# Kernel tuning notes

Measured on AMD Instinct MI355X. Metric: run time of the kernel, lower is better.

The kernel has to match this reference:

```python
import jax, jax.numpy as jnp
import numpy as np

EPS = 1e-5
TOP_K = 50

def _layernorm(h, g, b):
    mu = jnp.mean(h, axis=-1, keepdims=True)
    var = jnp.mean((h - mu) ** 2, axis=-1, keepdims=True)
    return (h - mu) * jax.lax.rsqrt(var + EPS) * g + b

def setup_inputs() -> dict:
    key = jax.random.key(0)
    ks = jax.random.split(key, 8)
    B, D, E = 16384, 384, 2048
    return {
        "x": jax.random.normal(ks[0], (B, D), jnp.float32),
        "We": jax.random.normal(ks[1], (D, E), jnp.float32) * 0.05,
        "be": jax.random.normal(ks[2], (E,), jnp.float32) * 0.01,
        "g1": jnp.ones((E,), jnp.float32),
        "b1": jnp.zeros((E,), jnp.float32),
        "Wd": jax.random.normal(ks[3], (E, D), jnp.float32) * 0.02,
        "bd": jax.random.normal(ks[4], (D,), jnp.float32) * 0.01,
        "Wb": jax.random.normal(ks[5], (E, D), jnp.float32) * 0.02,
        "bb": jax.random.normal(ks[6], (D,), jnp.float32) * 0.01,
        "g2": jnp.ones((D,), jnp.float32),
        "b2": jnp.zeros((D,), jnp.float32),
    }

def reference(x, We, be, g1, b1, Wd, bd, Wb, bb, g2, b2):
    # encoder: Linear -> LayerNorm -> ReLU
    h = jax.nn.relu(_layernorm(x @ We + be, g1, b1))  # [B, E]
    # top-k sparsification: zero all but top-50 per row (scatter mask, matches torch)
    _, idx = jax.lax.top_k(h, TOP_K)                  # [B, K]
    rows = jnp.arange(h.shape[0])[:, None]
    mask = jnp.zeros_like(h).at[rows, idx].set(1.0)
    sparse = h * mask                                 # [B, E]
    recon = sparse @ Wd + bd                          # [B, D]
    separated = _layernorm(sparse @ Wb + bb, g2, b2)  # [B, D]
    return recon, sparse, separated
```

## Files before the change

kernel.cpp:

```cpp
#include <hip/hip_runtime.h>
#include <hip/hip_bf16.h>
#include <stdint.h>

#define B_D   384
#define B_E   2048
#define TOPK  50
#define LN_EPS 1e-5f
#define NKP   12
#define FIX_WINDOW 2e-4f

typedef short bf16x8 __attribute__((ext_vector_type(8)));
typedef float f32x4  __attribute__((ext_vector_type(4)));

__device__ __forceinline__ float wave_sum_f(float v) {
#pragma unroll
    for (int d = 1; d < 64; d <<= 1) v += __shfl_xor(v, d, 64);
    return v;
}
__device__ __forceinline__ int wave_sum_i(int v) {
#pragma unroll
    for (int d = 1; d < 64; d <<= 1) v += __shfl_xor(v, d, 64);
    return v;
}
__device__ __forceinline__ float wave_max_f(float v) {
#pragma unroll
    for (int d = 1; d < 64; d <<= 1) v = fmaxf(v, __shfl_xor(v, d, 64));
    return v;
}

__device__ __forceinline__ ushort f2bf_hi(float v) {
    __hip_bfloat16 b = __float2bfloat16(v);
    return *(ushort*)&b;
}
__device__ __forceinline__ ushort f2bf_lo(float v) {
    __hip_bfloat16 b = __float2bfloat16(v);
    float rem = v - __bfloat162float(b);
    __hip_bfloat16 l = __float2bfloat16(rem);
    return *(ushort*)&l;
}

__device__ __forceinline__ void llds16(const void* g, void* l) {
    __builtin_amdgcn_global_load_lds((const __attribute__((address_space(1))) void*)g,
                                     (__attribute__((address_space(3))) void*)l, 16, 0, 0);
}

__global__ __launch_bounds__(256) void pack_AB(
    const float* __restrict__ x, const float* __restrict__ We,
    ushort* __restrict__ Ap, ushort* __restrict__ Bp, int* __restrict__ cntr)
{
    const int ks = blockIdx.x, yb = blockIdx.y, t = threadIdx.x;
    if (cntr && t == 0 && ks == 0 && yb == 0) *cntr = 0;
    if (yb < 64) {
        const int mt = yb;
#pragma unroll
        for (int q = 0; q < 8; ++q) {
            const int s = q * 256 + t;
            const int m = s & 255, kg = s >> 8;
            const int kp = ks * 64 + kg * 8;
            const int hi = (kp < 384);
            const int ksrc = hi ? kp : kp - 384;
            const float* src = x + (size_t)(mt * 256 + m) * B_D + ksrc;
            float4 v0 = *(const float4*)src;
            float4 v1 = *(const float4*)(src + 4);
            float vv[8] = {v0.x, v0.y, v0.z, v0.w, v1.x, v1.y, v1.z, v1.w};
            ushort o[8];
#pragma unroll
            for (int e = 0; e < 8; ++e)
                o[e] = hi ? f2bf_hi(vv[e]) : f2bf_lo(vv[e]);
            *(uint4*)(Ap + ((size_t)(mt * NKP + ks) * 2048 + s) * 8) = *(uint4*)o;
        }
    } else {
        const int nt = yb - 64;
#pragma unroll
        for (int q = 0; q < 8; ++q) {
            const int s = q * 256 + t;
            const int nl = s & 255, kg = s >> 8;
            const int kp = ks * 64 + kg * 8;
            const int hi = (kp < 384);
            const int ksrc = hi ? kp : kp - 384;
            const int ng = nt * 256 + nl;
            ushort o[8];
#pragma unroll
            for (int e = 0; e < 8; ++e) {
                float v = We[(size_t)(ksrc + e) * B_E + ng];
                o[e] = hi ? f2bf_hi(v) : f2bf_lo(v);
            }
            *(uint4*)(Bp + ((size_t)(nt * NKP + ks) * 2048 + s) * 8) = *(uint4*)o;
        }
    }
}

__global__ __launch_bounds__(512, 2) void enc_mfma256b(
    const ushort* __restrict__ Ap, const ushort* __restrict__ Bp,
    const float* __restrict__ be, float* __restrict__ y)
{
    __shared__ __align__(16) ushort Ah[2][8192];
    __shared__ __align__(16) ushort Al[2][8192];
    __shared__ __align__(16) ushort Bh[2][8192];
    __shared__ __align__(16) ushort Bl[2][8192];
    const int t = threadIdx.x, lane = t & 63, w = t >> 6;
    const int wr = w >> 2, wc = w & 3;
    const int gid = blockIdx.x;
    const int swz = (gid & 7) * 64 + (gid >> 3);
    const int nt = swz & 7, mt = swz >> 3;
    const ushort* gA = Ap + (size_t)mt * NKP * 16384;
    const ushort* gB = Bp + (size_t)nt * NKP * 16384;

    f32x4 acc[8][4];
#pragma unroll
    for (int i = 0; i < 8; ++i)
#pragma unroll
        for (int j = 0; j < 4; ++j)
#pragma unroll
            for (int r = 0; r < 4; ++r) acc[i][j][r] = 0.f;

    const int l15 = lane & 15, l4 = lane >> 4;

#define STAGEH(hk_, b_)                                                         \
    {                                                                           \
        const int hh = (hk_);                                                   \
        const int kt = hh >> 1, hf = hh & 1;                                    \
        const ushort* ah_ = gA + (size_t)kt * 16384 + hf * 8192 + t * 8;        \
        const ushort* al_ = gA + (size_t)(kt + 6) * 16384 + hf * 8192 + t * 8;  \
        const ushort* bh_ = gB + (size_t)kt * 16384 + hf * 8192 + t * 8;        \
        const ushort* bl_ = gB + (size_t)(kt + 6) * 16384 + hf * 8192 + t * 8;  \
        llds16(ah_,        &Ah[b_][t * 8]);                                     \
        llds16(ah_ + 4096, &Ah[b_][4096 + t * 8]);                              \
        llds16(al_,        &Al[b_][t * 8]);                                     \
        llds16(al_ + 4096, &Al[b_][4096 + t * 8]);                              \
        llds16(bh_,        &Bh[b_][t * 8]);                                     \
        llds16(bh_ + 4096, &Bh[b_][4096 + t * 8]);                              \
        llds16(bl_,        &Bl[b_][t * 8]);                                     \
        llds16(bl_ + 4096, &Bl[b_][4096 + t * 8]);                              \
    }

    STAGEH(0, 0);
    __syncthreads();

    for (int hk = 0; hk < 12; ++hk) {
        const int sl = hk & 1;
        if (hk + 1 < 12) STAGEH(hk + 1, sl ^ 1);
        bf16x8 bhf[4], ahf[8];
#pragma unroll
        for (int j = 0; j < 4; ++j)
            bhf[j] = *(const bf16x8*)&Bh[sl][(l4 * 256 + wc * 64 + j * 16 + l15) * 8];
#pragma unroll
        for (int i = 0; i < 8; ++i)
            ahf[i] = *(const bf16x8*)&Ah[sl][(l4 * 256 + wr * 128 + i * 16 + l15) * 8];
#pragma unroll
        for (int i = 0; i < 8; ++i)
#pragma unroll
            for (int j = 0; j < 4; ++j)
                acc[i][j] = __builtin_amdgcn_mfma_f32_16x16x32_bf16(ahf[i], bhf[j], acc[i][j], 0, 0, 0);
        bf16x8 blf[4];
#pragma unroll
        for (int j = 0; j < 4; ++j)
            blf[j] = *(const bf16x8*)&Bl[sl][(l4 * 256 + wc * 64 + j * 16 + l15) * 8];
#pragma unroll
        for (int i = 0; i < 8; ++i)
#pragma unroll
            for (int j = 0; j < 4; ++j)
                acc[i][j] = __builtin_amdgcn_mfma_f32_16x16x32_bf16(ahf[i], blf[j], acc[i][j], 0, 0, 0);
        bf16x8 alf[8];
#pragma unroll
        for (int i = 0; i < 8; ++i)
            alf[i] = *(const bf16x8*)&Al[sl][(l4 * 256 + wr * 128 + i * 16 + l15) * 8];
#pragma unroll
        for (int i = 0; i < 8; ++i)
#pragma unroll
            for (int j = 0; j < 4; ++j)
                acc[i][j] = __builtin_amdgcn_mfma_f32_16x16x32_bf16(alf[i], bhf[j], acc[i][j], 0, 0, 0);
        if (hk + 1 < 12) __syncthreads();
    }
#undef STAGEH

    float bev[4];
#pragma unroll
    for (int j = 0; j < 4; ++j) bev[j] = be[nt * 256 + wc * 64 + j * 16 + l15];
#pragma unroll
    for (int i = 0; i < 8; ++i)
#pragma unroll
        for (int j = 0; j < 4; ++j)
#pragma unroll
            for (int r = 0; r < 4; ++r) {
                const int row = mt * 256 + wr * 128 + i * 16 + l4 * 4 + r;
                const int col = nt * 256 + wc * 64 + j * 16 + l15;
                y[(size_t)row * B_E + col] = acc[i][j][r] + bev[j];
            }
}

__global__ __launch_bounds__(256) void enc_gemm_f32(
    const float* __restrict__ x, const float* __restrict__ We,
    const float* __restrict__ be, float* __restrict__ y)
{
    __shared__ float As[8][128];
    __shared__ float Bs[8][128];
    const int t  = threadIdx.x;
    const int m0 = blockIdx.y * 128;
    const int n0 = blockIdx.x * 128;
    const int tx = t & 15, ty = t >> 4;
    const int la_m = t >> 1, la_k = (t & 1) * 4;
    const int lb_k = t >> 5, lb_c = (t & 31) * 4;

    float acc[8][8];
#pragma unroll
    for (int i = 0; i < 8; ++i)
#pragma unroll
        for (int j = 0; j < 8; ++j) acc[i][j] = 0.f;

    for (int k0 = 0; k0 < B_D; k0 += 8) {
        float4 a = *(const float4*)&x[(size_t)(m0 + la_m) * B_D + k0 + la_k];
        float4 b = *(const float4*)&We[(size_t)(k0 + lb_k) * B_E + n0 + lb_c];
        __syncthreads();
        As[la_k + 0][la_m] = a.x;
        As[la_k + 1][la_m] = a.y;
        As[la_k + 2][la_m] = a.z;
        As[la_k + 3][la_m] = a.w;
        *(float4*)&Bs[lb_k][lb_c] = b;
        __syncthreads();
#pragma unroll
        for (int kk = 0; kk < 8; ++kk) {
            float4 a0 = *(const float4*)&As[kk][ty * 4];
            float4 a1 = *(const float4*)&As[kk][ty * 4 + 64];
            float4 b0 = *(const float4*)&Bs[kk][tx * 4];
            float4 b1 = *(const float4*)&Bs[kk][tx * 4 + 64];
            float av[8] = {a0.x,a0.y,a0.z,a0.w,a1.x,a1.y,a1.z,a1.w};
            float bv[8] = {b0.x,b0.y,b0.z,b0.w,b1.x,b1.y,b1.z,b1.w};
#pragma unroll
            for (int i = 0; i < 8; ++i)
#pragma unroll
                for (int j = 0; j < 8; ++j)
                    acc[i][j] = fmaf(av[i], bv[j], acc[i][j]);
        }
    }
    float4 beL = *(const float4*)&be[n0 + tx * 4];
    float4 beH = *(const float4*)&be[n0 + 64 + tx * 4];
    float bl[8] = {beL.x,beL.y,beL.z,beL.w,beH.x,beH.y,beH.z,beH.w};
#pragma unroll
    for (int i = 0; i < 8; ++i) {
        int row = m0 + ty * 4 + (i & 3) + (i >> 2) * 64;
        float4 o0 = {acc[i][0]+bl[0], acc[i][1]+bl[1], acc[i][2]+bl[2], acc[i][3]+bl[3]};
        float4 o1 = {acc[i][4]+bl[4], acc[i][5]+bl[5], acc[i][6]+bl[6], acc[i][7]+bl[7]};
        *(float4*)&y[(size_t)row * B_E + n0 + tx * 4]      = o0;
        *(float4*)&y[(size_t)row * B_E + n0 + 64 + tx * 4] = o1;
    }
}

__device__ __forceinline__ int ln_topk_row(
    float (&h)[32], int lane, const float* __restrict__ g1, const float* __restrict__ b1,
    float* __restrict__ row, int* __restrict__ IwR, float* __restrict__ VwR,
    float* __restrict__ ldsv, int* __restrict__ ldsi)
{
    float s = 0.f;
#pragma unroll
    for (int j = 0; j < 32; ++j) s += h[j];
    s = wave_sum_f(s);
    const float mu = s * (1.f / B_E);
    float ss = 0.f;
#pragma unroll
    for (int j = 0; j < 32; ++j) { float d = h[j] - mu; ss += d * d; }
    ss = wave_sum_f(ss);
    const float rstd = rsqrtf(ss * (1.f / B_E) + LN_EPS);
#pragma unroll
    for (int q = 0; q < 8; ++q) {
        float4 g  = *(const float4*)&g1[q * 256 + lane * 4];
        float4 bb = *(const float4*)&b1[q * 256 + lane * 4];
        float gg[4]  = {g.x,g.y,g.z,g.w};
        float bbv[4] = {bb.x,bb.y,bb.z,bb.w};
#pragma unroll
        for (int i = 0; i < 4; ++i) {
            int j = q*4+i;
            h[j] = fmaxf(fmaf((h[j] - mu) * rstd, gg[i], bbv[i]), 0.f);
        }
    }
    float mx = h[0];
#pragma unroll
    for (int j = 1; j < 32; ++j) mx = fmaxf(mx, h[j]);
    mx = wave_max_f(mx);

    float vlo = 0.f, vhi = __uint_as_float(__float_as_uint(mx) + 1u);
    int cl = 2048;
    bool window = false;
    for (int it = 0; it < 20; ++it) {
        float mid = 0.5f * (vlo + vhi);
        if (it == 0 && 2.2f > vlo && 2.2f < vhi) mid = 2.2f;
        if (!(mid > vlo && mid < vhi)) break;
        int c = 0;
#pragma unroll
        for (int j = 0; j < 32; ++j)
            c += (int)__popcll(__ballot(h[j] >= mid));
        if (c >= TOPK) { vlo = mid; cl = c; if (c <= 64) { window = true; break; } }
        else vhi = mid;
    }
    unsigned lo = __float_as_uint(vlo);
    if (!window) {
        unsigned hi = __float_as_uint(vhi);
        while (hi - lo > 1u) {
            const unsigned mid = lo + ((hi - lo) >> 1);
            const float mf = __uint_as_float(mid);
            int c = 0;
#pragma unroll
            for (int j = 0; j < 32; ++j)
                c += (int)__popcll(__ballot(h[j] >= mf));
            if (c >= TOPK) { lo = mid; cl = c; if (c <= 64) break; }
            else hi = mid;
        }
    }
    const float T0 = __uint_as_float(lo);

    unsigned selmask = 0u;
    int flag = 0;
    bool fastSel = (cl <= 64 && T0 > 0.f);

    if (fastSel) {
        ldsv[lane] = -1.f;
        ldsi[lane] = 1 << 20;
        asm volatile("s_waitcnt lgkmcnt(0)" ::: "memory");
        int base = 0;
#pragma unroll
        for (int j = 0; j < 32; ++j) {
            const bool p = (h[j] >= T0);
            const unsigned long long m = __ballot(p);
            if (p) {
                const int pos = base + (int)__popcll(m & ((1ull << lane) - 1ull));
                ldsv[pos] = h[j];
                ldsi[pos] = (j >> 2) * 256 + lane * 4 + (j & 3);
            }
            base += (int)__popcll(m);
        }
        asm volatile("s_waitcnt lgkmcnt(0)" ::: "memory");
        float sv = ldsv[lane];
        int   si = ldsi[lane];
#pragma unroll
        for (int k = 2; k <= 64; k <<= 1) {
#pragma unroll
            for (int jj = k >> 1; jj > 0; jj >>= 1) {
                const float ov = __shfl_xor(sv, jj, 64);
                const int   oi = __shfl_xor(si, jj, 64);
                const bool dirUp = ((lane & k) == 0);
                const bool lower = ((lane & jj) == 0);
                const bool mineBefore = (sv > ov) || (sv == ov && si < oi);
                const bool keep = (lower == dirUp) ? mineBefore : !mineBefore;
                if (!keep) { sv = ov; si = oi; }
            }
        }
        const float T    = __shfl(sv, TOPK - 1, 64);
        const int   idxT = __shfl(si, TOPK - 1, 64);
        float v51;
        if (cl > TOPK) {
            v51 = __shfl(sv, TOPK, 64);
        } else {
            float bb = -1.f;
#pragma unroll
            for (int j = 0; j < 32; ++j) bb = (h[j] < T0) ? fmaxf(bb, h[j]) : bb;
            v51 = wave_max_f(bb);
        }
        flag = (T - v51 < FIX_WINDOW) ? 1 : 0;
#pragma unroll
        for (int j = 0; j < 32; ++j) {
            const int e = (j >> 2) * 256 + lane * 4 + (j & 3);
            if (h[j] > T || (h[j] == T && e <= idxT)) selmask |= (1u << j);
        }
        if (lane < TOPK) { IwR[lane] = si; VwR[lane] = sv; }
    } else {
        const float T = T0;
        int cgt = 0, ceq = 0;
        float below = -1.f;
#pragma unroll
        for (int j = 0; j < 32; ++j) {
            cgt += (h[j] > T); ceq += (h[j] == T);
            if (h[j] < T) below = fmaxf(below, h[j]);
        }
        const int cgt_t = wave_sum_i(cgt);
        const int ceq_t = wave_sum_i(ceq);
        below = wave_max_f(below);
        const int need = TOPK - cgt_t;

        if (cgt_t + ceq_t == TOPK) {
#pragma unroll
            for (int j = 0; j < 32; ++j) if (h[j] >= T) selmask |= (1u << j);
        } else {
            int base = 0;
            for (int q = 0; q < 8; ++q) {
                int tc = 0;
#pragma unroll
                for (int i = 0; i < 4; ++i) tc += (h[q*4+i] == T);
                int ip = tc;
#pragma unroll
                for (int d = 1; d < 64; d <<= 1) {
                    int o = __shfl_up(ip, d, 64);
                    if (lane >= d) ip += o;
                }
                int rk  = base + ip - tc;
                int tot = __shfl(ip, 63, 64);
#pragma unroll
                for (int i = 0; i < 4; ++i) {
                    int j = q*4+i;
                    if (h[j] > T) selmask |= (1u << j);
                    else if (h[j] == T) { if (rk < need) selmask |= (1u << j); rk++; }
                }
                base += tot;
            }
        }
        if (T > 0.f) {
            if (cgt_t + ceq_t != TOPK && ceq_t > need) flag = 1;
            else if (T - below < FIX_WINDOW) flag = 1;
        }
        const int myc = __popc(selmask);
        int ip = myc;
#pragma unroll
        for (int d = 1; d < 64; d <<= 1) {
            int o = __shfl_up(ip, d, 64);
            if (lane >= d) ip += o;
        }
        int pos = ip - myc;
        for (int j = 0; j < 32; ++j) {
            if ((selmask >> j) & 1u) {
                int e = (j >> 2) * 256 + lane * 4 + (j & 3);
                IwR[pos] = e;
                VwR[pos] = h[j];
                pos++;
            }
        }
    }

#pragma unroll
    for (int q = 0; q < 8; ++q) {
        float4 o;
        o.x = ((selmask >> (q*4+0)) & 1u) ? h[q*4+0] : 0.f;
        o.y = ((selmask >> (q*4+1)) & 1u) ? h[q*4+1] : 0.f;
        o.z = ((selmask >> (q*4+2)) & 1u) ? h[q*4+2] : 0.f;
        o.w = ((selmask >> (q*4+3)) & 1u) ? h[q*4+3] : 0.f;
        *(float4*)&row[q * 256 + lane * 4] = o;
    }
    return flag;
}

__global__ __launch_bounds__(256) void topk_packW(
    float* __restrict__ y, const float* __restrict__ g1, const float* __restrict__ b1,
    int* __restrict__ Iw, float* __restrict__ Vw,
    int* __restrict__ rowlist, int* __restrict__ cntr,
    const float* __restrict__ Wd, const float* __restrict__ Wb, uint* __restrict__ Wp,
    int nTopk)
{
    __shared__ float ldsv[4][64];
    __shared__ int   ldsi[4][64];
    const int bid = blockIdx.x;
    const int t = threadIdx.x;
    if (bid >= nTopk) {
        const int e = (bid - nTopk) * 2 + (t >> 7);
        const int tt = t & 127;
#pragma unroll
        for (int j = 0; j < 3; ++j) {
            const int c = tt + 128 * j;
            const ushort d = f2bf_hi(Wd[(size_t)e * B_D + c]);
            const ushort b = f2bf_hi(Wb[(size_t)e * B_D + c]);
            Wp[(size_t)e * B_D + c] = ((uint)b << 16) | (uint)d;
        }
        return;
    }
    const int lane = t & 63;
    const int w = t >> 6;
    const int r = bid * 4 + w;
    float* row = y + (size_t)r * B_E;
    float h[32];
#pragma unroll
    for (int q = 0; q < 8; ++q) {
        float4 v = *(const float4*)&row[q * 256 + lane * 4];
        h[q*4+0] = v.x; h[q*4+1] = v.y; h[q*4+2] = v.z; h[q*4+3] = v.w;
    }
    int flag = ln_topk_row(h, lane, g1, b1, row, Iw + r * TOPK, Vw + r * TOPK,
                           ldsv[w], ldsi[w]);
    if (rowlist && lane == 0 && flag) {
        int p = atomicAdd(cntr, 1);
        rowlist[p] = r;
    }
}

__global__ __launch_bounds__(256) void fixup_recompute(
    const float* __restrict__ x, const float* __restrict__ We, const float* __restrict__ be,
    float* __restrict__ y, const int* __restrict__ rowlist, const int* __restrict__ cntr)
{
    const int nflag = *cntr;
    const int t = threadIdx.x;
    __shared__ float xs[8][B_D];
    __shared__ int   rIdx[8];

    for (int rb = blockIdx.y * 8; rb < nflag; rb += gridDim.y * 8) {
        const int nact = min(nflag - rb, 8);
        __syncthreads();
        if (t < 8) rIdx[t] = (t < nact) ? rowlist[rb + t] : -1;
        __syncthreads();
#pragma unroll
        for (int i = 0; i < 8; ++i) {
            if (i < nact) {
                const float* src = x + (size_t)rIdx[i] * B_D;
                for (int j = t; j < B_D; j += 256) xs[i][j] = src[j];
            } else {
                for (int j = t; j < B_D; j += 256) xs[i][j] = 0.f;
            }
        }
        __syncthreads();

        const int c = blockIdx.x * 256 + t;
        const float bc = be[c];
        float acc[8];
#pragma unroll
        for (int i = 0; i < 8; ++i) acc[i] = bc;
#pragma unroll 4
        for (int k = 0; k < B_D; ++k) {
            const float w = We[(size_t)k * B_E + c];
#pragma unroll
            for (int i = 0; i < 8; ++i) acc[i] = fmaf(xs[i][k], w, acc[i]);
        }
#pragma unroll
        for (int i = 0; i < 8; ++i)
            if (i < nact) y[(size_t)rIdx[i] * B_E + c] = acc[i];
    }
}

__global__ __launch_bounds__(256) void fixup_select(
    float* __restrict__ y, const float* __restrict__ g1, const float* __restrict__ b1,
    int* __restrict__ Iw, float* __restrict__ Vw,
    const int* __restrict__ rowlist, const int* __restrict__ cntr)
{
    __shared__ float ldsv[4][64];
    __shared__ int   ldsi[4][64];
    const int nflag = *cntr;
    const int w = threadIdx.x >> 6;
    const int lane = threadIdx.x & 63;
    for (int i = blockIdx.x * 4 + w; i < nflag; i += gridDim.x * 4) {
        const int r = rowlist[i];
        float* row = y + (size_t)r * B_E;
        float h[32];
#pragma unroll
        for (int q = 0; q < 8; ++q) {
            float4 v = *(const float4*)&row[q * 256 + lane * 4];
            h[q*4+0] = v.x; h[q*4+1] = v.y; h[q*4+2] = v.z; h[q*4+3] = v.w;
        }
        ln_topk_row(h, lane, g1, b1, row, Iw + r * TOPK, Vw + r * TOPK,
                    ldsv[w], ldsi[w]);
    }
}

__global__ __launch_bounds__(512) void decode_packed4(
    const int* __restrict__ Iw, const float* __restrict__ Vw,
    const uint* __restrict__ Wp, const float* __restrict__ bd,
    const float* __restrict__ bbias, const float* __restrict__ g2,
    const float* __restrict__ b2, float* __restrict__ recon, float* __restrict__ sep)
{
    __shared__ int   sI[4][TOPK];
    __shared__ float sV[4][TOPK];
    __shared__ float red[4][2];
    const int q = threadIdx.x >> 7;
    const int t = threadIdx.x & 127;
    const int r = blockIdx.x * 4 + q;
    if (t < TOPK) { sI[q][t] = Iw[r * TOPK + t]; sV[q][t] = Vw[r * TOPK + t]; }
    __syncthreads();
    float ad[3], ab[3];
#pragma unroll
    for (int j = 0; j < 3; ++j) { ad[j] = bd[t + 128*j]; ab[j] = bbias[t + 128*j]; }
#pragma unroll 2
    for (int i = 0; i < TOPK; ++i) {
        const int   idx = sI[q][i];
        const float v   = sV[q][i];
        const uint* wp  = Wp + (size_t)idx * B_D;
#pragma unroll
        for (int j = 0; j < 3; ++j) {
            const uint u = wp[t + 128*j];
            const float wd = __uint_as_float(u << 16);
            const float wb = __uint_as_float(u & 0xFFFF0000u);
            ad[j] = fmaf(v, wd, ad[j]);
            ab[j] = fmaf(v, wb, ab[j]);
        }
    }
#pragma unroll
    for (int j = 0; j < 3; ++j) recon[(size_t)r * B_D + t + 128*j] = ad[j];
    float s = ab[0] + ab[1] + ab[2];
    s = wave_sum_f(s);
    if ((t & 63) == 0) red[q][t >> 6] = s;
    __syncthreads();
    const float mu = (red[q][0] + red[q][1]) * (1.f / B_D);
    __syncthreads();
    float ss = 0.f;
#pragma unroll
    for (int j = 0; j < 3; ++j) { float d = ab[j] - mu; ss += d * d; }
    ss = wave_sum_f(ss);
    if ((t & 63) == 0) red[q][t >> 6] = ss;
    __syncthreads();
    const float rstd = rsqrtf((red[q][0] + red[q][1]) * (1.f / B_D) + LN_EPS);
#pragma unroll
    for (int j = 0; j < 3; ++j) {
        int c = t + 128*j;
        sep[(size_t)r * B_D + c] = fmaf((ab[j] - mu) * rstd, g2[c], b2[c]);
    }
}

__global__ __launch_bounds__(128) void decode_f32(
    const int* __restrict__ Iw, const float* __restrict__ Vw,
    const float* __restrict__ Wd, const float* __restrict__ bd,
    const float* __restrict__ Wb, const float* __restrict__ bbias,
    const float* __restrict__ g2, const float* __restrict__ b2,
    float* __restrict__ recon, float* __restrict__ sep)
{
    __shared__ int   sI[TOPK];
    __shared__ float sV[TOPK];
    __shared__ float red[2];
    const int r = blockIdx.x, t = threadIdx.x;
    if (t < TOPK) { sI[t] = Iw[r * TOPK + t]; sV[t] = Vw[r * TOPK + t]; }
    __syncthreads();
    float ad[3], ab[3];
#pragma unroll
    for (int j = 0; j < 3; ++j) { ad[j] = bd[t + 128*j]; ab[j] = bbias[t + 128*j]; }
#pragma unroll 2
    for (int i = 0; i < TOPK; ++i) {
        const int   idx = sI[i];
        const float v   = sV[i];
        const float* wd = Wd + (size_t)idx * B_D;
        const float* wb = Wb + (size_t)idx * B_D;
#pragma unroll
        for (int j = 0; j < 3; ++j) {
            ad[j] = fmaf(v, wd[t + 128*j], ad[j]);
            ab[j] = fmaf(v, wb[t + 128*j], ab[j]);
        }
    }
#pragma unroll
    for (int j = 0; j < 3; ++j) recon[(size_t)r * B_D + t + 128*j] = ad[j];
    float s = ab[0] + ab[1] + ab[2];
    s = wave_sum_f(s);
    if ((t & 63) == 0) red[t >> 6] = s;
    __syncthreads();
    const float mu = (red[0] + red[1]) * (1.f / B_D);
    __syncthreads();
    float ss = 0.f;
#pragma unroll
    for (int j = 0; j < 3; ++j) { float d = ab[j] - mu; ss += d * d; }
    ss = wave_sum_f(ss);
    if ((t & 63) == 0) red[t >> 6] = ss;
    __syncthreads();
    const float rstd = rsqrtf((red[0] + red[1]) * (1.f / B_D) + LN_EPS);
#pragma unroll
    for (int j = 0; j < 3; ++j) {
        int c = t + 128*j;
        sep[(size_t)r * B_D + c] = fmaf((ab[j] - mu) * rstd, g2[c], b2[c]);
    }
}

__global__ __launch_bounds__(256) void topk_only(
    float* __restrict__ y, const float* __restrict__ g1, const float* __restrict__ b1,
    int* __restrict__ Iw, float* __restrict__ Vw)
{
    __shared__ float ldsv[4][64];
    __shared__ int   ldsi[4][64];
    const int lane = threadIdx.x & 63;
    const int w = threadIdx.x >> 6;
    const int r = blockIdx.x * 4 + w;
    float* row = y + (size_t)r * B_E;
    float h[32];
#pragma unroll
    for (int q = 0; q < 8; ++q) {
        float4 v = *(const float4*)&row[q * 256 + lane * 4];
        h[q*4+0] = v.x; h[q*4+1] = v.y; h[q*4+2] = v.z; h[q*4+3] = v.w;
    }
    ln_topk_row(h, lane, g1, b1, row, Iw + r * TOPK, Vw + r * TOPK, ldsv[w], ldsi[w]);
}

extern "C" void kernel_launch(void* const* d_in, const int* in_sizes, int n_in,
                              void* d_out, int out_size, void* d_ws, size_t ws_size,
                              hipStream_t stream)
{
    const float* x  = (const float*)d_in[0];
    const float* We = (const float*)d_in[1];
    const float* be = (const float*)d_in[2];
    const float* g1 = (const float*)d_in[3];
    const float* b1 = (const float*)d_in[4];
    const float* Wd = (const float*)d_in[5];
    const float* bd = (const float*)d_in[6];
    const float* Wb = (const float*)d_in[7];
    const float* bb = (const float*)d_in[8];
    const float* g2 = (const float*)d_in[9];
    const float* b2 = (const float*)d_in[10];

    const int Brows = in_sizes[0] / B_D;
    float* recon  = (float*)d_out;
    float* sparse = recon + (size_t)Brows * B_D;
    float* sep    = sparse + (size_t)Brows * B_E;

    char* ws = (char*)d_ws;
    int*   Iw      = (int*)ws;
    float* Vw      = (float*)(ws + 3276800);
    int*   rowlist = (int*)(ws + 6619136);
    int*   cntr    = (int*)(ws + 6684672);
    const size_t apOff = 6688768;
    const size_t bpOff = apOff + (size_t)64 * NKP * 2048 * 16;
    const size_t need  = bpOff + (size_t)8 * NKP * 2048 * 16;

    if (ws_size >= need) {
        ushort* Ap = (ushort*)(ws + apOff);
        ushort* Bp = (ushort*)(ws + bpOff);
        uint*   Wp = (uint*)(ws + apOff);
        pack_AB<<<dim3(NKP, 72), dim3(256), 0, stream>>>(x, We, Ap, Bp, cntr);
        enc_mfma256b<<<dim3(512), dim3(512), 0, stream>>>(Ap, Bp, be, sparse);
        topk_packW<<<dim3(Brows / 4 + 1024), dim3(256), 0, stream>>>(
            sparse, g1, b1, Iw, Vw, rowlist, cntr, Wd, Wb, Wp, Brows / 4);
        fixup_recompute<<<dim3(8, 64), dim3(256), 0, stream>>>(x, We, be, sparse, rowlist, cntr);
        fixup_select<<<dim3(256), dim3(256), 0, stream>>>(sparse, g1, b1, Iw, Vw, rowlist, cntr);
        decode_packed4<<<dim3(Brows / 4), dim3(512), 0, stream>>>(Iw, Vw, Wp, bd, bb, g2, b2, recon, sep);
    } else {
        enc_gemm_f32<<<dim3(16, 128), dim3(256), 0, stream>>>(x, We, be, sparse);
        topk_only<<<dim3(Brows / 4), dim3(256), 0, stream>>>(sparse, g1, b1, Iw, Vw);
        decode_f32<<<dim3(Brows), dim3(128), 0, stream>>>(Iw, Vw, Wd, bd, Wb, bb, g2, b2, recon, sep);
    }
}
```

Before: 266.8 us.

## Fuse fixup top-k reselection into decode kernel with one wave per row

Removes the separate fixup_select launch and folds its work into the decode kernel. A per-row flag array tells decode whether to redo LN+top-k, and the selected indices and values then go to each lane through LDS and wave shuffles. Decode now maps one 64-lane wave per row with 6 columns per lane, which removes the block-level __syncthreads reductions. In exchange it adds a flags read per row, and flagged rows get serial top-k work inside the decode blocks.

```diff
diff --git a/kernel.cpp b/kernel.cpp
--- a/kernel.cpp
+++ b/kernel.cpp
@@ -362,6 +362,8 @@
             if (h[j] > T || (h[j] == T && e <= idxT)) selmask |= (1u << j);
         }
         if (lane < TOPK) { IwR[lane] = si; VwR[lane] = sv; }
+        ldsv[lane] = sv;
+        ldsi[lane] = si;
     } else {
         const float T = T0;
         int cgt = 0, ceq = 0;
@@ -419,6 +421,8 @@
                 int e = (j >> 2) * 256 + lane * 4 + (j & 3);
                 IwR[pos] = e;
                 VwR[pos] = h[j];
+                ldsi[pos] = e;
+                ldsv[pos] = h[j];
                 pos++;
             }
         }
@@ -433,13 +437,14 @@
         o.w = ((selmask >> (q*4+3)) & 1u) ? h[q*4+3] : 0.f;
         *(float4*)&row[q * 256 + lane * 4] = o;
     }
+    asm volatile("s_waitcnt lgkmcnt(0)" ::: "memory");
     return flag;
 }
 
 __global__ __launch_bounds__(256) void topk_packW(
     float* __restrict__ y, const float* __restrict__ g1, const float* __restrict__ b1,
     int* __restrict__ Iw, float* __restrict__ Vw,
-    int* __restrict__ rowlist, int* __restrict__ cntr,
+    int* __restrict__ flags, int* __restrict__ rowlist, int* __restrict__ cntr,
     const float* __restrict__ Wd, const float* __restrict__ Wb, uint* __restrict__ Wp,
     int nTopk)
 {
@@ -471,9 +476,12 @@
     }
     int flag = ln_topk_row(h, lane, g1, b1, row, Iw + r * TOPK, Vw + r * TOPK,
                            ldsv[w], ldsi[w]);
-    if (rowlist && lane == 0 && flag) {
-        int p = atomicAdd(cntr, 1);
-        rowlist[p] = r;
+    if (lane == 0) {
+        flags[r] = flag;
+        if (flag) {
+            int p = atomicAdd(cntr, 1);
+            rowlist[p] = r;
+        }
     }
 }
 
@@ -519,18 +527,21 @@
     }
 }
 
-__global__ __launch_bounds__(256) void fixup_select(
+__global__ __launch_bounds__(256) void decode_fused(
     float* __restrict__ y, const float* __restrict__ g1, const float* __restrict__ b1,
-    int* __restrict__ Iw, float* __restrict__ Vw,
-    const int* __restrict__ rowlist, const int* __restrict__ cntr)
+    int* __restrict__ Iw, float* __restrict__ Vw, const int* __restrict__ flags,
+    const uint* __restrict__ Wp, const float* __restrict__ bd,
+    const float* __restrict__ bbias, const float* __restrict__ g2,
+    const float* __restrict__ b2, float* __restrict__ recon, float* __restrict__ sep)
 {
     __shared__ float ldsv[4][64];
     __shared__ int   ldsi[4][64];
-    const int nflag = *cntr;
-    const int w = threadIdx.x >> 6;
-    const int lane = threadIdx.x & 63;
-    for (int i = blockIdx.x * 4 + w; i < nflag; i += gridDim.x * 4) {
-        const int r = rowlist[i];
+    const int w = threadIdx.x >> 6, lane = threadIdx.x & 63;
+    const int r = blockIdx.x * 4 + w;
+
+    int   iv = 0;
+    float vv = 0.f;
+    if (flags[r]) {
         float* row = y + (size_t)r * B_E;
         float h[32];
 #pragma unroll
@@ -540,34 +551,28 @@
         }
         ln_topk_row(h, lane, g1, b1, row, Iw + r * TOPK, Vw + r * TOPK,
                     ldsv[w], ldsi[w]);
-    }
-}
-
-__global__ __launch_bounds__(512) void decode_packed4(
-    const int* __restrict__ Iw, const float* __restrict__ Vw,
-    const uint* __restrict__ Wp, const float* __restrict__ bd,
-    const float* __restrict__ bbias, const float* __restrict__ g2,
-    const float* __restrict__ b2, float* __restrict__ recon, float* __restrict__ sep)
-{
-    __shared__ int   sI[4][TOPK];
-    __shared__ float sV[4][TOPK];
-    __shared__ float red[4][2];
-    const int q = threadIdx.x >> 7;
-    const int t = threadIdx.x & 127;
-    const int r = blockIdx.x * 4 + q;
-    if (t < TOPK) { sI[q][t] = Iw[r * TOPK + t]; sV[q][t] = Vw[r * TOPK + t]; }
-    __syncthreads();
-    float ad[3], ab[3];
-#pragma unroll
-    for (int j = 0; j < 3; ++j) { ad[j] = bd[t + 128*j]; ab[j] = bbias[t + 128*j]; }
+        iv = ldsi[w][lane];
+        vv = ldsv[w][lane];
+    } else if (lane < TOPK) {
+        iv = Iw[r * TOPK + lane];
+        vv = Vw[r * TOPK + lane];
+    }
+
+    float ad[6], ab[6];
+#pragma unroll
+    for (int j = 0; j < 6; ++j) {
+        const int c = j * 64 + lane;
+        ad[j] = bd[c];
+        ab[j] = bbias[c];
+    }
 #pragma unroll 2
     for (int i = 0; i < TOPK; ++i) {
-        const int   idx = sI[q][i];
-        const float v   = sV[q][i];
+        const int   idx = __shfl(iv, i, 64);
+        const float v   = __shfl(vv, i, 64);
         const uint* wp  = Wp + (size_t)idx * B_D;
 #pragma unroll
-        for (int j = 0; j < 3; ++j) {
-            const uint u = wp[t + 128*j];
+        for (int j = 0; j < 6; ++j) {
+            const uint u = wp[j * 64 + lane];
             const float wd = __uint_as_float(u << 16);
             const float wb = __uint_as_float(u & 0xFFFF0000u);
             ad[j] = fmaf(v, wd, ad[j]);
@@ -575,23 +580,20 @@
         }
     }
 #pragma unroll
-    for (int j = 0; j < 3; ++j) recon[(size_t)r * B_D + t + 128*j] = ad[j];
-    float s = ab[0] + ab[1] + ab[2];
+    for (int j = 0; j < 6; ++j) recon[(size_t)r * B_D + j * 64 + lane] = ad[j];
+    float s = 0.f;
+#pragma unroll
+    for (int j = 0; j < 6; ++j) s += ab[j];
     s = wave_sum_f(s);
-    if ((t & 63) == 0) red[q][t >> 6] = s;
-    __syncthreads();
-    const float mu = (red[q][0] + red[q][1]) * (1.f / B_D);
-    __syncthreads();
+    const float mu = s * (1.f / B_D);
     float ss = 0.f;
 #pragma unroll
-    for (int j = 0; j < 3; ++j) { float d = ab[j] - mu; ss += d * d; }
+    for (int j = 0; j < 6; ++j) { float d = ab[j] - mu; ss += d * d; }
     ss = wave_sum_f(ss);
-    if ((t & 63) == 0) red[q][t >> 6] = ss;
-    __syncthreads();
-    const float rstd = rsqrtf((red[q][0] + red[q][1]) * (1.f / B_D) + LN_EPS);
-#pragma unroll
-    for (int j = 0; j < 3; ++j) {
-        int c = t + 128*j;
+    const float rstd = rsqrtf(ss * (1.f / B_D) + LN_EPS);
+#pragma unroll
+    for (int j = 0; j < 6; ++j) {
+        const int c = j * 64 + lane;
         sep[(size_t)r * B_D + c] = fmaf((ab[j] - mu) * rstd, g2[c], b2[c]);
     }
 }
@@ -689,6 +691,7 @@
     char* ws = (char*)d_ws;
     int*   Iw      = (int*)ws;
     float* Vw      = (float*)(ws + 3276800);
+    int*   flags   = (int*)(ws + 6553600);
     int*   rowlist = (int*)(ws + 6619136);
     int*   cntr    = (int*)(ws + 6684672);
     const size_t apOff = 6688768;
@@ -702,10 +705,10 @@
         pack_AB<<<dim3(NKP, 72), dim3(256), 0, stream>>>(x, We, Ap, Bp, cntr);
         enc_mfma256b<<<dim3(512), dim3(512), 0, stream>>>(Ap, Bp, be, sparse);
         topk_packW<<<dim3(Brows / 4 + 1024), dim3(256), 0, stream>>>(
-            sparse, g1, b1, Iw, Vw, rowlist, cntr, Wd, Wb, Wp, Brows / 4);
+            sparse, g1, b1, Iw, Vw, flags, rowlist, cntr, Wd, Wb, Wp, Brows / 4);
         fixup_recompute<<<dim3(8, 64), dim3(256), 0, stream>>>(x, We, be, sparse, rowlist, cntr);
-        fixup_select<<<dim3(256), dim3(256), 0, stream>>>(sparse, g1, b1, Iw, Vw, rowlist, cntr);
-        decode_packed4<<<dim3(Brows / 4), dim3(512), 0, stream>>>(Iw, Vw, Wp, bd, bb, g2, b2, recon, sep);
+        decode_fused<<<dim3(Brows / 4), dim3(256), 0, stream>>>(
+            sparse, g1, b1, Iw, Vw, flags, Wp, bd, bb, g2, b2, recon, sep);
     } else {
         enc_gemm_f32<<<dim3(16, 128), dim3(256), 0, stream>>>(x, We, be, sparse);
         topk_only<<<dim3(Brows / 4), dim3(256), 0, stream>>>(sparse, g1, b1, Iw, Vw);
```

After: 258.5 us. -3.1%, faster.
